# Performance work log

Measured on AMD Instinct MI355X. Metric: run time of the kernel, lower is better.

The kernel has to match this reference:

```python
import jax, jax.numpy as jnp
import numpy as np

B, L, D = 1, 1024, 1024
NL = 4            # n_layers
N = 16            # d_state
DI = 2 * D        # d_inner (expand=2)
DTR = (D + 15) // 16  # dt_rank = ceil(d_model/16) = 64
K = 4             # depthwise conv kernel size
EPS = 1e-5


def setup_inputs() -> dict:
    key = jax.random.key(0)
    ks = jax.random.split(key, 8)
    s = lambda k, shp, sc: jax.random.normal(k, shp, jnp.float32) * sc
    x = s(ks[0], (B, L, D), 1.0)
    norm_w = jnp.ones((NL, D), jnp.float32)
    in_w = s(ks[1], (NL, 2 * DI, D), D ** -0.5)          # in_proj (no bias)
    conv_w = s(ks[2], (NL, DI, K), 0.5)                   # depthwise conv1d weight
    conv_b = s(ks[3], (NL, DI), 0.02)                     # conv1d bias
    xproj_w = s(ks[4], (NL, DTR + 2 * N, DI), DI ** -0.5) # x_proj (no bias)
    dt_w = s(ks[5], (NL, DI, DTR), DTR ** -0.5)           # dt_proj weight
    dt_b = jnp.full((NL, DI), 0.1, jnp.float32)           # dt_proj bias (positive-ish delta)
    A_log = jnp.log(jnp.tile(jnp.arange(1, N + 1, dtype=jnp.float32), (NL, DI, 1)))  # [NL, DI, N]
    D_skip = jnp.ones((NL, DI), jnp.float32)
    out_w = s(ks[6], (NL, D, DI), DI ** -0.5)             # out_proj (no bias)
    return dict(x=x, norm_w=norm_w, in_w=in_w, conv_w=conv_w, conv_b=conv_b,
                xproj_w=xproj_w, dt_w=dt_w, dt_b=dt_b, A_log=A_log,
                D_skip=D_skip, out_w=out_w)


def _rmsnorm(x, w):
    return x * jax.lax.rsqrt(jnp.mean(x * x, axis=-1, keepdims=True) + EPS) * w


def _causal_depthwise_conv(u, w, b):
    # u: [B, L, DI], w: [DI, K], b: [DI]; causal (left pad K-1)
    up = jnp.pad(u, ((0, 0), (K - 1, 0), (0, 0)))
    y = b
    for k in range(K):
        y = y + up[:, k:k + L, :] * w[:, k]
    return y


def _selective_scan(dA, dBu, C):
    # dA, dBu: [B, L, DI, N]; C: [B, L, N]
    def step(h, inp):
        a, bu, c = inp
        h = a * h + bu                       # [B, DI, N]
        y = jnp.einsum('bdn,bn->bd', h, c)   # [B, DI]
        return h, y
    h0 = jnp.zeros((dA.shape[0], DI, N), dA.dtype)
    _, ys = jax.lax.scan(step, h0, (dA.transpose(1, 0, 2, 3),
                                    dBu.transpose(1, 0, 2, 3),
                                    C.transpose(1, 0, 2)))
    return ys.transpose(1, 0, 2)             # [B, L, DI]


def _mamba_block(x, p):
    norm_w, in_w, conv_w, conv_b, xproj_w, dt_w, dt_b, A_log, D_skip, out_w = p
    xn = _rmsnorm(x, norm_w)
    xz = jnp.einsum('bld,ed->ble', xn, in_w)             # [B, L, 2*DI]
    u, z = jnp.split(xz, 2, axis=-1)
    u = jax.nn.silu(_causal_depthwise_conv(u, conv_w, conv_b))
    x_dbl = jnp.einsum('bld,ed->ble', u, xproj_w)        # [B, L, DTR+2N]
    dt_r, Bt, Ct = jnp.split(x_dbl, [DTR, DTR + N], axis=-1)
    delta = jax.nn.softplus(jnp.einsum('blr,dr->bld', dt_r, dt_w) + dt_b)  # [B, L, DI]
    A = -jnp.exp(A_log)                                  # [DI, N]
    dA = jnp.exp(delta[..., None] * A)                   # [B, L, DI, N]
    dBu = delta[..., None] * Bt[:, :, None, :] * u[..., None]
    y = _selective_scan(dA, dBu, Ct) + u * D_skip        # [B, L, DI]
    y = y * jax.nn.silu(z)
    return x + jnp.einsum('ble,de->bld', y, out_w)       # residual


def reference(x, norm_w, in_w, conv_w, conv_b, xproj_w, dt_w, dt_b, A_log, D_skip, out_w):
    params = (norm_w, in_w, conv_w, conv_b, xproj_w, dt_w, dt_b, A_log, D_skip, out_w)
    out, _ = jax.lax.scan(lambda h, p: (_mamba_block(h, p), None), x, params)
    return out
```

## Files before the change

### kernel.cpp

```cpp
#include <hip/hip_runtime.h>
#include <hip/hip_bf16.h>
#include <stdint.h>

#define L 1024
#define D 1024
#define NLAYER 4
#define NSTATE 16
#define DI 2048
#define DTR 64
#define KCONV 4
#define XD 96
#define NC 64
#define CT 16
#define KSPLIT 8
#define OSPLIT 4
#define BK 32
#define DIST 4

typedef __attribute__((ext_vector_type(8))) short short8;
typedef __attribute__((ext_vector_type(4))) float floatx4;

__device__ __forceinline__ float siluf(float x) { return x / (1.f + __expf(-x)); }

__device__ __forceinline__ unsigned short f2bf(float x) {
    __hip_bfloat16 b = __float2bfloat16(x);
    return *reinterpret_cast<unsigned short*>(&b);
}

__device__ __forceinline__ short8 pack8(floatx4 a, floatx4 b) {
    short8 o;
    o[0] = (short)f2bf(a.x); o[1] = (short)f2bf(a.y);
    o[2] = (short)f2bf(a.z); o[3] = (short)f2bf(a.w);
    o[4] = (short)f2bf(b.x); o[5] = (short)f2bf(b.y);
    o[6] = (short)f2bf(b.z); o[7] = (short)f2bf(b.w);
    return o;
}

#define BARRIER_NODRAIN() asm volatile("s_waitcnt lgkmcnt(0)\n\ts_barrier" ::: "memory")

__global__ __launch_bounds__(256) void rmsnorm_kernel(const float* __restrict__ x,
                                                      const float* __restrict__ w,
                                                      __hip_bfloat16* __restrict__ out) {
    int row = blockIdx.x;
    const float* xr = x + (size_t)row * D;
    float v[4];
    float s = 0.f;
#pragma unroll
    for (int i = 0; i < 4; ++i) {
        v[i] = xr[threadIdx.x + i * 256];
        s += v[i] * v[i];
    }
#pragma unroll
    for (int off = 32; off > 0; off >>= 1) s += __shfl_xor(s, off, 64);
    __shared__ float red[4];
    int wave = threadIdx.x >> 6;
    if ((threadIdx.x & 63) == 0) red[wave] = s;
    __syncthreads();
    float tot = red[0] + red[1] + red[2] + red[3];
    float inv = rsqrtf(tot * (1.f / D) + 1e-5f);
#pragma unroll
    for (int i = 0; i < 4; ++i) {
        int c = threadIdx.x + i * 256;
        out[(size_t)row * D + c] = __float2bfloat16(v[i] * inv * w[c]);
    }
}

template <int EPI, int ITERS>
__global__ __launch_bounds__(256, 2) void gemm_pipe(
    const __hip_bfloat16* __restrict__ A, int lda,
    const float* __restrict__ Bw, int ldb, int Brows,
    float* __restrict__ C, int ldc, int Nvalid,
    long zstride, const float* __restrict__ bias) {
    __shared__ __align__(16) __hip_bfloat16 As[2][128 * BK];
    __shared__ __align__(16) __hip_bfloat16 Bs[2][64 * BK];
    int tid = threadIdx.x;
    int wave = tid >> 6, lane = tid & 63;

    int gxy = gridDim.x * gridDim.y;
    int total = gxy * gridDim.z;
    int flat = (blockIdx.z * gridDim.y + blockIdx.y) * gridDim.x + blockIdx.x;
    int bm, bn, bz;
    if ((total & 7) == 0) {
        int lid = (flat & 7) * (total >> 3) + (flat >> 3);
        bz = lid / gxy;
        int rem = lid - bz * gxy;
        bn = rem / gridDim.y;
        bm = rem - bn * gridDim.y;
    } else {
        bm = blockIdx.y; bn = blockIdx.x; bz = blockIdx.z;
    }

    int m0 = bm * 128, n0 = bn * 64;
    int k_base = bz * (ITERS * BK);
    C += (long)bz * zstride;
    int wr = wave >> 1, wc = wave & 1;
    int srow = lane >> 2, scol = (lane & 3) * 8;
    int q = lane >> 4, r = lane & 15;

    floatx4 acc[4][2] = {};

    const __hip_bfloat16* gA0 = A + (long)(m0 + wave * 32 + srow) * lda + scol + k_base;
    const __hip_bfloat16* gA1 = gA0 + (long)16 * lda;
    int bnrow = n0 + wave * 16 + srow;
    const float* gB = Bw + (long)bnrow * ldb + scol + k_base;
    bool bok = bnrow < Brows;

    short8 qa0[DIST], qa1[DIST];
    floatx4 qb0[DIST] = {}, qb1[DIST] = {};

    auto ld = [&](int j) {
        int k0 = j * BK;
        int s = j & (DIST - 1);
        qa0[s] = *(const short8*)(gA0 + k0);
        qa1[s] = *(const short8*)(gA1 + k0);
        if (bok) {
            qb0[s] = *(const floatx4*)(gB + k0);
            qb1[s] = *(const floatx4*)(gB + k0 + 4);
        }
    };
    auto wrstage = [&](int j) {
        int p = j & 1, s = j & (DIST - 1);
        *(short8*)(&As[p][(wave * 32 + srow) * BK + scol]) = qa0[s];
        *(short8*)(&As[p][(wave * 32 + 16 + srow) * BK + scol]) = qa1[s];
        *(short8*)(&Bs[p][(wave * 16 + srow) * BK + scol]) = pack8(qb0[s], qb1[s]);
    };

#pragma unroll
    for (int j = 0; j < DIST; ++j)
        if (j < ITERS) ld(j);
    wrstage(0);

#pragma unroll
    for (int k = 0; k < ITERS; ++k) {
        BARRIER_NODRAIN();
        if (k + DIST < ITERS) ld(k + DIST);
        if (k + 1 < ITERS) wrstage(k + 1);
        const short* Ap = (const short*)As[k & 1];
        const short* Bp = (const short*)Bs[k & 1];
        short8 af[4], bfr[2];
#pragma unroll
        for (int i = 0; i < 4; ++i)
            af[i] = *(const short8*)(Ap + (wr * 64 + i * 16 + r) * BK + q * 8);
#pragma unroll
        for (int j = 0; j < 2; ++j)
            bfr[j] = *(const short8*)(Bp + (wc * 32 + j * 16 + r) * BK + q * 8);
#pragma unroll
        for (int i = 0; i < 4; ++i)
#pragma unroll
            for (int j = 0; j < 2; ++j)
                acc[i][j] = __builtin_amdgcn_mfma_f32_16x16x32_bf16(af[i], bfr[j], acc[i][j], 0, 0, 0);
    }

#pragma unroll
    for (int i = 0; i < 4; ++i) {
        int mrow = m0 + wr * 64 + i * 16 + q * 4;
#pragma unroll
        for (int j = 0; j < 2; ++j) {
            int ncol = n0 + wc * 32 + j * 16 + r;
            if (ncol < Nvalid) {
#pragma unroll
                for (int rr = 0; rr < 4; ++rr) {
                    float v = acc[i][j][rr];
                    int m = mrow + rr;
                    if (EPI == 1) {
                        v += bias[ncol];
                        v = v > 20.f ? v : log1pf(__expf(v));
                    }
                    C[(long)m * ldc + ncol] = v;
                }
            }
        }
    }
}

template <int ITERS>
__global__ __launch_bounds__(256, 1) void gemm128(
    const __hip_bfloat16* __restrict__ A, int lda,
    const float* __restrict__ Bw, int ldb, int Brows,
    float* __restrict__ C, int ldc,
    long zstride) {
    __shared__ __align__(16) __hip_bfloat16 As[2][128 * BK];
    __shared__ __align__(16) __hip_bfloat16 Bs[2][128 * BK];
    int tid = threadIdx.x;
    int wave = tid >> 6, lane = tid & 63;

    int gxy = gridDim.x * gridDim.y;
    int total = gxy * gridDim.z;
    int flat = (blockIdx.z * gridDim.y + blockIdx.y) * gridDim.x + blockIdx.x;
    int bm, bn, bz;
    if ((total & 7) == 0) {
        int lid = (flat & 7) * (total >> 3) + (flat >> 3);
        bz = lid / gxy;
        int rem = lid - bz * gxy;
        bn = rem / gridDim.y;
        bm = rem - bn * gridDim.y;
    } else {
        bm = blockIdx.y; bn = blockIdx.x; bz = blockIdx.z;
    }

    int m0 = bm * 128, n0 = bn * 128;
    int k_base = bz * (ITERS * BK);
    C += (long)bz * zstride;
    int wr = wave >> 1, wc = wave & 1;
    int srow = lane >> 2, scol = (lane & 3) * 8;
    int q = lane >> 4, r = lane & 15;

    floatx4 acc[4][4] = {};

    const __hip_bfloat16* gA0 = A + (long)(m0 + wave * 32 + srow) * lda + scol + k_base;
    const __hip_bfloat16* gA1 = gA0 + (long)16 * lda;
    int bn0 = n0 + wave * 32 + srow;
    const float* gB0 = Bw + (long)bn0 * ldb + scol + k_base;
    const float* gB1 = gB0 + (long)16 * ldb;
    bool bok0 = bn0 < Brows, bok1 = (bn0 + 16) < Brows;

    short8 qa0[DIST], qa1[DIST];
    floatx4 qb0[DIST] = {}, qb1[DIST] = {}, qb2[DIST] = {}, qb3[DIST] = {};

    auto ld = [&](int j) {
        int k0 = j * BK;
        int s = j & (DIST - 1);
        qa0[s] = *(const short8*)(gA0 + k0);
        qa1[s] = *(const short8*)(gA1 + k0);
        if (bok0) {
            qb0[s] = *(const floatx4*)(gB0 + k0);
            qb1[s] = *(const floatx4*)(gB0 + k0 + 4);
        }
        if (bok1) {
            qb2[s] = *(const floatx4*)(gB1 + k0);
            qb3[s] = *(const floatx4*)(gB1 + k0 + 4);
        }
    };
    auto wrstage = [&](int j) {
        int p = j & 1, s = j & (DIST - 1);
        *(short8*)(&As[p][(wave * 32 + srow) * BK + scol]) = qa0[s];
        *(short8*)(&As[p][(wave * 32 + 16 + srow) * BK + scol]) = qa1[s];
        *(short8*)(&Bs[p][(wave * 32 + srow) * BK + scol]) = pack8(qb0[s], qb1[s]);
        *(short8*)(&Bs[p][(wave * 32 + 16 + srow) * BK + scol]) = pack8(qb2[s], qb3[s]);
    };

#pragma unroll
    for (int j = 0; j < DIST; ++j)
        if (j < ITERS) ld(j);
    wrstage(0);

#pragma unroll
    for (int k = 0; k < ITERS; ++k) {
        BARRIER_NODRAIN();
        if (k + DIST < ITERS) ld(k + DIST);
        if (k + 1 < ITERS) wrstage(k + 1);
        const short* Ap = (const short*)As[k & 1];
        const short* Bp = (const short*)Bs[k & 1];
        short8 af[4], bfr[4];
#pragma unroll
        for (int i = 0; i < 4; ++i)
            af[i] = *(const short8*)(Ap + (wr * 64 + i * 16 + r) * BK + q * 8);
#pragma unroll
        for (int j = 0; j < 4; ++j)
            bfr[j] = *(const short8*)(Bp + (wc * 64 + j * 16 + r) * BK + q * 8);
#pragma unroll
        for (int i = 0; i < 4; ++i)
#pragma unroll
            for (int j = 0; j < 4; ++j)
                acc[i][j] = __builtin_amdgcn_mfma_f32_16x16x32_bf16(af[i], bfr[j], acc[i][j], 0, 0, 0);
    }

#pragma unroll
    for (int i = 0; i < 4; ++i) {
        int mrow = m0 + wr * 64 + i * 16 + q * 4;
#pragma unroll
        for (int j = 0; j < 4; ++j) {
            int ncol = n0 + wc * 64 + j * 16 + r;
#pragma unroll
            for (int rr = 0; rr < 4; ++rr)
                C[(long)(mrow + rr) * ldc + ncol] = acc[i][j][rr];
        }
    }
}

template <int NPART, bool NORM>
__global__ __launch_bounds__(256) void reduce_kernel(const float* __restrict__ part2,
                                                     const float* __restrict__ xin,
                                                     const float* __restrict__ nw,
                                                     float* __restrict__ out,
                                                     __hip_bfloat16* __restrict__ xn) {
    int row = blockIdx.x;
    const float* xr = xin + (size_t)row * D;
    float v[4];
    float ss = 0.f;
#pragma unroll
    for (int i = 0; i < 4; ++i) {
        int c = threadIdx.x + i * 256;
        float s = xr[c];
#pragma unroll
        for (int p = 0; p < NPART; ++p)
            s += part2[(size_t)p * L * D + (size_t)row * D + c];
        v[i] = s;
        out[(size_t)row * D + c] = s;
        ss += s * s;
    }
    if (NORM) {
#pragma unroll
        for (int off = 32; off > 0; off >>= 1) ss += __shfl_xor(ss, off, 64);
        __shared__ float red[4];
        int wave = threadIdx.x >> 6;
        if ((threadIdx.x & 63) == 0) red[wave] = ss;
        __syncthreads();
        float inv = rsqrtf((red[0] + red[1] + red[2] + red[3]) * (1.f / D) + 1e-5f);
#pragma unroll
        for (int i = 0; i < 4; ++i) {
            int c = threadIdx.x + i * 256;
            xn[(size_t)row * D + c] = __float2bfloat16(v[i] * inv * nw[c]);
        }
    }
}

__global__ __launch_bounds__(256) void conv_silu_kernel(const float* __restrict__ xz,
                                                        const float* __restrict__ cw,
                                                        const float* __restrict__ cb,
                                                        __hip_bfloat16* __restrict__ u) {
    int idx = blockIdx.x * 256 + threadIdx.x;
    int d = idx & (DI - 1);
    int t = idx >> 11;
    float acc = cb[d];
#pragma unroll
    for (int k = 0; k < KCONV; ++k) {
        int tk = t - (KCONV - 1) + k;
        if (tk >= 0) acc += xz[(size_t)tk * (2 * DI) + d] * cw[d * KCONV + k];
    }
    u[idx] = __float2bfloat16(siluf(acc));
}

__global__ __launch_bounds__(256) void xred_kernel(const float* __restrict__ part,
                                                   __hip_bfloat16* __restrict__ xdbl_bf,
                                                   float* __restrict__ xdblBC) {
    int i = blockIdx.x * 256 + threadIdx.x;
    int t = i / XD, col = i - t * XD;
    float s = 0.f;
#pragma unroll
    for (int sp = 0; sp < KSPLIT; ++sp) s += part[(size_t)sp * L * XD + i];
    if (col < DTR) xdbl_bf[(size_t)t * DTR + col] = __float2bfloat16(s);
    else xdblBC[(size_t)t * 32 + (col - DTR)] = s;
}

__global__ __launch_bounds__(256) void scanA_kernel(const float* __restrict__ delta,
                                                    const __hip_bfloat16* __restrict__ u,
                                                    const float* __restrict__ xdblBC,
                                                    const float* __restrict__ Alog,
                                                    float* __restrict__ Ach,
                                                    float* __restrict__ Bch) {
    int d = blockIdx.x * 256 + threadIdx.x;
    int c = blockIdx.y;
    __shared__ __align__(16) float Bsh[CT * NSTATE];
    int tt0 = threadIdx.x >> 4, c0 = threadIdx.x & 15;
    Bsh[threadIdx.x] = xdblBC[(size_t)(c * CT + tt0) * 32 + c0];
    __syncthreads();

    float aval[NSTATE];
    const float4* Al4 = (const float4*)(Alog + (size_t)d * NSTATE);
#pragma unroll
    for (int n4 = 0; n4 < 4; ++n4) {
        float4 t = Al4[n4];
        aval[n4 * 4 + 0] = -__expf(t.x);
        aval[n4 * 4 + 1] = -__expf(t.y);
        aval[n4 * 4 + 2] = -__expf(t.z);
        aval[n4 * 4 + 3] = -__expf(t.w);
    }
    float h[NSTATE], ap[NSTATE];
#pragma unroll
    for (int n = 0; n < NSTATE; ++n) { h[n] = 0.f; ap[n] = 1.f; }

    for (int tt = 0; tt < CT; ++tt) {
        int t = c * CT + tt;
        float dl = delta[(size_t)t * DI + d];
        float uu = __bfloat162float(u[(size_t)t * DI + d]);
        float du = dl * uu;
        const float4* Bv = (const float4*)(Bsh + tt * NSTATE);
#pragma unroll
        for (int n4 = 0; n4 < 4; ++n4) {
            float4 b = Bv[n4];
            float bb[4] = {b.x, b.y, b.z, b.w};
#pragma unroll
            for (int k = 0; k < 4; ++k) {
                int n = n4 * 4 + k;
                float a = __expf(dl * aval[n]);
                h[n] = a * h[n] + du * bb[k];
                ap[n] *= a;
            }
        }
    }
    float4* Ao = (float4*)(Ach + ((size_t)c * DI + d) * NSTATE);
    float4* Bo = (float4*)(Bch + ((size_t)c * DI + d) * NSTATE);
#pragma unroll
    for (int n4 = 0; n4 < 4; ++n4) {
        Ao[n4] = make_float4(ap[n4 * 4], ap[n4 * 4 + 1], ap[n4 * 4 + 2], ap[n4 * 4 + 3]);
        Bo[n4] = make_float4(h[n4 * 4], h[n4 * 4 + 1], h[n4 * 4 + 2], h[n4 * 4 + 3]);
    }
}

__global__ __launch_bounds__(256) void scanB_kernel(float* __restrict__ Ach,
                                                    const float* __restrict__ Bch) {
    long i = blockIdx.x * 256 + threadIdx.x;
    const long S = (long)DI * NSTATE;
    constexpr int P = 8;
    float ab[P], bb[P];
#pragma unroll
    for (int j = 0; j < P; ++j) {
        ab[j] = Ach[(long)j * S + i];
        bb[j] = Bch[(long)j * S + i];
    }
    float h = 0.f;
#pragma unroll
    for (int c = 0; c < NC; ++c) {
        float a = ab[c & (P - 1)];
        float b = bb[c & (P - 1)];
        Ach[(long)c * S + i] = h;
        if (c + P < NC) {
            ab[c & (P - 1)] = Ach[(long)(c + P) * S + i];
            bb[c & (P - 1)] = Bch[(long)(c + P) * S + i];
        }
        h = a * h + b;
    }
}

__global__ __launch_bounds__(256) void scanC_kernel(const float* __restrict__ delta,
                                                    const __hip_bfloat16* __restrict__ u,
                                                    const float* __restrict__ xdblBC,
                                                    const float* __restrict__ Alog,
                                                    const float* __restrict__ Hin,
                                                    const float* __restrict__ xz,
                                                    const float* __restrict__ Dskip,
                                                    __hip_bfloat16* __restrict__ yg) {
    int d = blockIdx.x * 256 + threadIdx.x;
    int c = blockIdx.y;
    __shared__ __align__(16) float Bsh[CT * NSTATE];
    __shared__ __align__(16) float Csh[CT * NSTATE];
    int tt0 = threadIdx.x >> 4, c0 = threadIdx.x & 15;
    Bsh[threadIdx.x] = xdblBC[(size_t)(c * CT + tt0) * 32 + c0];
    Csh[threadIdx.x] = xdblBC[(size_t)(c * CT + tt0) * 32 + 16 + c0];
    __syncthreads();

    float aval[NSTATE];
    const float4* Al4 = (const float4*)(Alog + (size_t)d * NSTATE);
#pragma unroll
    for (int n4 = 0; n4 < 4; ++n4) {
        float4 t = Al4[n4];
        aval[n4 * 4 + 0] = -__expf(t.x);
        aval[n4 * 4 + 1] = -__expf(t.y);
        aval[n4 * 4 + 2] = -__expf(t.z);
        aval[n4 * 4 + 3] = -__expf(t.w);
    }
    float h[NSTATE];
    const float4* Hi = (const float4*)(Hin + ((size_t)c * DI + d) * NSTATE);
#pragma unroll
    for (int n4 = 0; n4 < 4; ++n4) {
        float4 t = Hi[n4];
        h[n4 * 4 + 0] = t.x; h[n4 * 4 + 1] = t.y; h[n4 * 4 + 2] = t.z; h[n4 * 4 + 3] = t.w;
    }
    float dsk = Dskip[d];

    for (int tt = 0; tt < CT; ++tt) {
        int t = c * CT + tt;
        float dl = delta[(size_t)t * DI + d];
        float uu = __bfloat162float(u[(size_t)t * DI + d]);
        float du = dl * uu;
        const float4* Bv = (const float4*)(Bsh + tt * NSTATE);
        const float4* Cv = (const float4*)(Csh + tt * NSTATE);
        float y = 0.f;
#pragma unroll
        for (int n4 = 0; n4 < 4; ++n4) {
            float4 b = Bv[n4];
            float4 cc = Cv[n4];
            float bb[4] = {b.x, b.y, b.z, b.w};
            float cv[4] = {cc.x, cc.y, cc.z, cc.w};
#pragma unroll
            for (int k = 0; k < 4; ++k) {
                int n = n4 * 4 + k;
                float a = __expf(dl * aval[n]);
                h[n] = a * h[n] + du * bb[k];
                y += h[n] * cv[k];
            }
        }
        float z = xz[(size_t)t * (2 * DI) + DI + d];
        yg[(size_t)t * DI + d] = __float2bfloat16((y + uu * dsk) * siluf(z));
    }
}

extern "C" void kernel_launch(void* const* d_in, const int* in_sizes, int n_in,
                              void* d_out, int out_size, void* d_ws, size_t ws_size,
                              hipStream_t stream) {
    const float* x      = (const float*)d_in[0];
    const float* norm_w = (const float*)d_in[1];
    const float* in_w   = (const float*)d_in[2];
    const float* conv_w = (const float*)d_in[3];
    const float* conv_b = (const float*)d_in[4];
    const float* xproj_w= (const float*)d_in[5];
    const float* dt_w   = (const float*)d_in[6];
    const float* dt_b   = (const float*)d_in[7];
    const float* A_log  = (const float*)d_in[8];
    const float* D_skip = (const float*)d_in[9];
    const float* out_w  = (const float*)d_in[10];
    float* out = (float*)d_out;

    uint8_t* wp = (uint8_t*)d_ws;
    auto alloc = [&](size_t bytes) {
        uint8_t* p = wp;
        wp += (bytes + 255) & ~(size_t)255;
        return p;
    };
    __hip_bfloat16* xn_bf   = (__hip_bfloat16*)alloc((size_t)L * D * 2);
    float*          xz      = (float*)alloc((size_t)L * 2 * DI * 4);
    __hip_bfloat16* u_bf    = (__hip_bfloat16*)alloc((size_t)L * DI * 2);
    float*          part    = (float*)alloc((size_t)KSPLIT * L * XD * 4);
    __hip_bfloat16* xdbl_bf = (__hip_bfloat16*)alloc((size_t)L * DTR * 2);
    float*          xdblBC  = (float*)alloc((size_t)L * 32 * 4);
    float*          delta   = (float*)alloc((size_t)L * DI * 4);
    __hip_bfloat16* yg_bf   = (__hip_bfloat16*)alloc((size_t)L * DI * 2);
    float*          part2   = (float*)alloc((size_t)OSPLIT * L * D * 4);
    float*          Ach     = (float*)alloc((size_t)NC * DI * NSTATE * 4);
    float*          Bch     = (float*)alloc((size_t)NC * DI * NSTATE * 4);

    rmsnorm_kernel<<<L, 256, 0, stream>>>(x, norm_w, xn_bf);

    for (int l = 0; l < NLAYER; ++l) {
        const float* xin = (l == 0) ? x : out;

        gemm128<32><<<dim3(4096 / 128, L / 128, 1), 256, 0, stream>>>(
            xn_bf, D, in_w + (size_t)l * 4096 * 1024, D, 4096,
            xz, 4096, 0);

        conv_silu_kernel<<<L * DI / 256, 256, 0, stream>>>(
            xz, conv_w + (size_t)l * DI * KCONV, conv_b + (size_t)l * DI, u_bf);

        gemm_pipe<0, 8><<<dim3(2, L / 128, KSPLIT), 256, 0, stream>>>(
            u_bf, DI, xproj_w + (size_t)l * 96 * 2048, DI, 96,
            part, XD, XD, (long)L * XD, nullptr);
        xred_kernel<<<(L * XD) / 256, 256, 0, stream>>>(part, xdbl_bf, xdblBC);

        gemm_pipe<1, 2><<<dim3(2048 / 64, L / 128, 1), 256, 0, stream>>>(
            xdbl_bf, DTR, dt_w + (size_t)l * 2048 * 64, DTR, 2048,
            delta, DI, DI, 0, dt_b + (size_t)l * DI);

        scanA_kernel<<<dim3(DI / 256, NC), 256, 0, stream>>>(
            delta, u_bf, xdblBC, A_log + (size_t)l * DI * NSTATE, Ach, Bch);
        scanB_kernel<<<(DI * NSTATE) / 256, 256, 0, stream>>>(Ach, Bch);
        scanC_kernel<<<dim3(DI / 256, NC), 256, 0, stream>>>(
            delta, u_bf, xdblBC, A_log + (size_t)l * DI * NSTATE, Ach, xz,
            D_skip + (size_t)l * DI, yg_bf);

        gemm128<16><<<dim3(1024 / 128, L / 128, OSPLIT), 256, 0, stream>>>(
            yg_bf, DI, out_w + (size_t)l * 1024 * 2048, DI, 1024,
            part2, D, (long)L * D);

        if (l < NLAYER - 1)
            reduce_kernel<OSPLIT, true><<<L, 256, 0, stream>>>(
                part2, xin, norm_w + (size_t)(l + 1) * D, out, xn_bf);
        else
            reduce_kernel<OSPLIT, false><<<L, 256, 0, stream>>>(
                part2, xin, nullptr, out, nullptr);
    }
}
```

Before: 598.7 us.

## Replace three-pass chunked selective scan with single sequential fused scan kernel

Replaces the chunked scan (a per-chunk local scan, a cross-chunk carry pass and a re-scan with output) with one kernel. Each block owns 32 channels and walks all 1024 timesteps in order, with 8 lanes per channel each holding 2 states. Delta, u, z and B/C are double-buffered through LDS in 64-step tiles, and lanes are reduced with shuffles. This removes the redundant exponentials, the Ach/Bch traffic and two launches. In exchange only 64 blocks run and each carries a long serial dependency chain, so the scan becomes latency-bound with low occupancy.

After: 1.230 ms. 2.05x slower.

```diff
diff --git a/kernel.cpp b/kernel.cpp
--- a/kernel.cpp
+++ b/kernel.cpp
@@ -10,12 +10,12 @@
 #define DTR 64
 #define KCONV 4
 #define XD 96
-#define NC 64
-#define CT 16
 #define KSPLIT 8
 #define OSPLIT 4
 #define BK 32
 #define DIST 4
+#define SCAND 32
+#define TT 64
 
 typedef __attribute__((ext_vector_type(8))) short short8;
 typedef __attribute__((ext_vector_type(4))) float floatx4;
@@ -56,8 +56,7 @@
     int wave = threadIdx.x >> 6;
     if ((threadIdx.x & 63) == 0) red[wave] = s;
     __syncthreads();
-    float tot = red[0] + red[1] + red[2] + red[3];
-    float inv = rsqrtf(tot * (1.f / D) + 1e-5f);
+    float inv = rsqrtf((red[0] + red[1] + red[2] + red[3]) * (1.f / D) + 1e-5f);
 #pragma unroll
     for (int i = 0; i < 4; ++i) {
         int c = threadIdx.x + i * 256;
@@ -177,8 +176,7 @@
 __global__ __launch_bounds__(256, 1) void gemm128(
     const __hip_bfloat16* __restrict__ A, int lda,
     const float* __restrict__ Bw, int ldb, int Brows,
-    float* __restrict__ C, int ldc,
-    long zstride) {
+    float* __restrict__ C, int ldc, long zstride) {
     __shared__ __align__(16) __hip_bfloat16 As[2][128 * BK];
     __shared__ __align__(16) __hip_bfloat16 Bs[2][128 * BK];
     int tid = threadIdx.x;
@@ -343,146 +341,82 @@
     else xdblBC[(size_t)t * 32 + (col - DTR)] = s;
 }
 
-__global__ __launch_bounds__(256) void scanA_kernel(const float* __restrict__ delta,
-                                                    const __hip_bfloat16* __restrict__ u,
-                                                    const float* __restrict__ xdblBC,
-                                                    const float* __restrict__ Alog,
-                                                    float* __restrict__ Ach,
-                                                    float* __restrict__ Bch) {
-    int d = blockIdx.x * 256 + threadIdx.x;
-    int c = blockIdx.y;
-    __shared__ __align__(16) float Bsh[CT * NSTATE];
-    int tt0 = threadIdx.x >> 4, c0 = threadIdx.x & 15;
-    Bsh[threadIdx.x] = xdblBC[(size_t)(c * CT + tt0) * 32 + c0];
-    __syncthreads();
-
-    float aval[NSTATE];
-    const float4* Al4 = (const float4*)(Alog + (size_t)d * NSTATE);
-#pragma unroll
-    for (int n4 = 0; n4 < 4; ++n4) {
-        float4 t = Al4[n4];
-        aval[n4 * 4 + 0] = -__expf(t.x);
-        aval[n4 * 4 + 1] = -__expf(t.y);
-        aval[n4 * 4 + 2] = -__expf(t.z);
-        aval[n4 * 4 + 3] = -__expf(t.w);
-    }
-    float h[NSTATE], ap[NSTATE];
-#pragma unroll
-    for (int n = 0; n < NSTATE; ++n) { h[n] = 0.f; ap[n] = 1.f; }
-
-    for (int tt = 0; tt < CT; ++tt) {
-        int t = c * CT + tt;
-        float dl = delta[(size_t)t * DI + d];
-        float uu = __bfloat162float(u[(size_t)t * DI + d]);
-        float du = dl * uu;
-        const float4* Bv = (const float4*)(Bsh + tt * NSTATE);
-#pragma unroll
-        for (int n4 = 0; n4 < 4; ++n4) {
-            float4 b = Bv[n4];
-            float bb[4] = {b.x, b.y, b.z, b.w};
-#pragma unroll
-            for (int k = 0; k < 4; ++k) {
-                int n = n4 * 4 + k;
-                float a = __expf(dl * aval[n]);
-                h[n] = a * h[n] + du * bb[k];
-                ap[n] *= a;
-            }
-        }
-    }
-    float4* Ao = (float4*)(Ach + ((size_t)c * DI + d) * NSTATE);
-    float4* Bo = (float4*)(Bch + ((size_t)c * DI + d) * NSTATE);
-#pragma unroll
-    for (int n4 = 0; n4 < 4; ++n4) {
-        Ao[n4] = make_float4(ap[n4 * 4], ap[n4 * 4 + 1], ap[n4 * 4 + 2], ap[n4 * 4 + 3]);
-        Bo[n4] = make_float4(h[n4 * 4], h[n4 * 4 + 1], h[n4 * 4 + 2], h[n4 * 4 + 3]);
-    }
-}
-
-__global__ __launch_bounds__(256) void scanB_kernel(float* __restrict__ Ach,
-                                                    const float* __restrict__ Bch) {
-    long i = blockIdx.x * 256 + threadIdx.x;
-    const long S = (long)DI * NSTATE;
-    constexpr int P = 8;
-    float ab[P], bb[P];
-#pragma unroll
-    for (int j = 0; j < P; ++j) {
-        ab[j] = Ach[(long)j * S + i];
-        bb[j] = Bch[(long)j * S + i];
-    }
-    float h = 0.f;
-#pragma unroll
-    for (int c = 0; c < NC; ++c) {
-        float a = ab[c & (P - 1)];
-        float b = bb[c & (P - 1)];
-        Ach[(long)c * S + i] = h;
-        if (c + P < NC) {
-            ab[c & (P - 1)] = Ach[(long)(c + P) * S + i];
-            bb[c & (P - 1)] = Bch[(long)(c + P) * S + i];
-        }
-        h = a * h + b;
-    }
-}
-
-__global__ __launch_bounds__(256) void scanC_kernel(const float* __restrict__ delta,
-                                                    const __hip_bfloat16* __restrict__ u,
-                                                    const float* __restrict__ xdblBC,
-                                                    const float* __restrict__ Alog,
-                                                    const float* __restrict__ Hin,
-                                                    const float* __restrict__ xz,
-                                                    const float* __restrict__ Dskip,
-                                                    __hip_bfloat16* __restrict__ yg) {
-    int d = blockIdx.x * 256 + threadIdx.x;
-    int c = blockIdx.y;
-    __shared__ __align__(16) float Bsh[CT * NSTATE];
-    __shared__ __align__(16) float Csh[CT * NSTATE];
-    int tt0 = threadIdx.x >> 4, c0 = threadIdx.x & 15;
-    Bsh[threadIdx.x] = xdblBC[(size_t)(c * CT + tt0) * 32 + c0];
-    Csh[threadIdx.x] = xdblBC[(size_t)(c * CT + tt0) * 32 + 16 + c0];
-    __syncthreads();
-
-    float aval[NSTATE];
-    const float4* Al4 = (const float4*)(Alog + (size_t)d * NSTATE);
-#pragma unroll
-    for (int n4 = 0; n4 < 4; ++n4) {
-        float4 t = Al4[n4];
-        aval[n4 * 4 + 0] = -__expf(t.x);
-        aval[n4 * 4 + 1] = -__expf(t.y);
-        aval[n4 * 4 + 2] = -__expf(t.z);
-        aval[n4 * 4 + 3] = -__expf(t.w);
-    }
-    float h[NSTATE];
-    const float4* Hi = (const float4*)(Hin + ((size_t)c * DI + d) * NSTATE);
-#pragma unroll
-    for (int n4 = 0; n4 < 4; ++n4) {
-        float4 t = Hi[n4];
-        h[n4 * 4 + 0] = t.x; h[n4 * 4 + 1] = t.y; h[n4 * 4 + 2] = t.z; h[n4 * 4 + 3] = t.w;
-    }
-    float dsk = Dskip[d];
-
-    for (int tt = 0; tt < CT; ++tt) {
-        int t = c * CT + tt;
-        float dl = delta[(size_t)t * DI + d];
-        float uu = __bfloat162float(u[(size_t)t * DI + d]);
-        float du = dl * uu;
-        const float4* Bv = (const float4*)(Bsh + tt * NSTATE);
-        const float4* Cv = (const float4*)(Csh + tt * NSTATE);
-        float y = 0.f;
-#pragma unroll
-        for (int n4 = 0; n4 < 4; ++n4) {
-            float4 b = Bv[n4];
-            float4 cc = Cv[n4];
-            float bb[4] = {b.x, b.y, b.z, b.w};
-            float cv[4] = {cc.x, cc.y, cc.z, cc.w};
-#pragma unroll
-            for (int k = 0; k < 4; ++k) {
-                int n = n4 * 4 + k;
-                float a = __expf(dl * aval[n]);
-                h[n] = a * h[n] + du * bb[k];
-                y += h[n] * cv[k];
-            }
-        }
-        float z = xz[(size_t)t * (2 * DI) + DI + d];
-        yg[(size_t)t * DI + d] = __float2bfloat16((y + uu * dsk) * siluf(z));
+__global__ __launch_bounds__(256) void scan1_kernel(
+    const float* __restrict__ delta, const __hip_bfloat16* __restrict__ u,
+    const float* __restrict__ xdblBC, const float* __restrict__ Alog,
+    const float* __restrict__ xz, const float* __restrict__ Dskip,
+    __hip_bfloat16* __restrict__ yg) {
+    const int d0 = blockIdx.x * SCAND;
+    const int tid = threadIdx.x;
+    const int dl_ = tid >> 3;
+    const int ng = tid & 7;
+    const int d = d0 + dl_;
+    const int n0 = ng * 2;
+
+    __shared__ __align__(16) float dsl[2][TT * SCAND];
+    __shared__ __align__(16) float usl[2][TT * SCAND];
+    __shared__ __align__(16) float zsl[2][TT * SCAND];
+    __shared__ __align__(16) float bcs[2][TT * 32];
+    __shared__ __align__(16) float ysl[TT * SCAND];
+    __shared__ float dskL[SCAND];
+
+    if (tid < SCAND) dskL[tid] = Dskip[d0 + tid];
+
+    float av0 = -__expf(Alog[(size_t)d * NSTATE + n0]);
+    float av1 = -__expf(Alog[(size_t)d * NSTATE + n0 + 1]);
+    float h0 = 0.f, h1 = 0.f;
+
+    auto stage = [&](int b, int tile) {
+        int T0 = tile * TT;
+#pragma unroll
+        for (int i = 0; i < (TT * SCAND) / 256; ++i) {
+            int idx = i * 256 + tid;
+            int tt = idx >> 5, col = idx & 31;
+            int t = T0 + tt;
+            dsl[b][idx] = delta[(size_t)t * DI + d0 + col];
+            usl[b][idx] = __bfloat162float(u[(size_t)t * DI + d0 + col]);
+            zsl[b][idx] = xz[(size_t)t * (2 * DI) + DI + d0 + col];
+            bcs[b][idx] = xdblBC[(size_t)t * 32 + col];
+        }
+    };
+
+    stage(0, 0);
+    for (int tile = 0; tile < L / TT; ++tile) {
+        int b = tile & 1;
+        __syncthreads();
+        if (tile + 1 < L / TT) stage(b ^ 1, tile + 1);
+#pragma unroll 4
+        for (int tt = 0; tt < TT; ++tt) {
+            float dlv = dsl[b][tt * SCAND + dl_];
+            float uu  = usl[b][tt * SCAND + dl_];
+            float du  = dlv * uu;
+            float bb0 = bcs[b][tt * 32 + n0];
+            float bb1 = bcs[b][tt * 32 + n0 + 1];
+            float cc0 = bcs[b][tt * 32 + 16 + n0];
+            float cc1 = bcs[b][tt * 32 + 16 + n0 + 1];
+            float a0 = __expf(dlv * av0);
+            float a1 = __expf(dlv * av1);
+            h0 = a0 * h0 + du * bb0;
+            h1 = a1 * h1 + du * bb1;
+            float y = h0 * cc0 + h1 * cc1;
+            y += __shfl_xor(y, 1);
+            y += __shfl_xor(y, 2);
+            y += __shfl_xor(y, 4);
+            if (ng == 0) ysl[tt * SCAND + dl_] = y;
+        }
+        __syncthreads();
+        int T0 = tile * TT;
+#pragma unroll
+        for (int i = 0; i < (TT * SCAND) / 256; ++i) {
+            int idx = i * 256 + tid;
+            int tt = idx >> 5, col = idx & 31;
+            int t = T0 + tt;
+            float y = ysl[idx];
+            float uu = usl[b][idx];
+            float z = zsl[b][idx];
+            yg[(size_t)t * DI + d0 + col] =
+                __float2bfloat16((y + uu * dskL[col]) * siluf(z));
+        }
     }
 }
 
@@ -517,8 +451,6 @@
     float*          delta   = (float*)alloc((size_t)L * DI * 4);
     __hip_bfloat16* yg_bf   = (__hip_bfloat16*)alloc((size_t)L * DI * 2);
     float*          part2   = (float*)alloc((size_t)OSPLIT * L * D * 4);
-    float*          Ach     = (float*)alloc((size_t)NC * DI * NSTATE * 4);
-    float*          Bch     = (float*)alloc((size_t)NC * DI * NSTATE * 4);
 
     rmsnorm_kernel<<<L, 256, 0, stream>>>(x, norm_w, xn_bf);
 
@@ -526,8 +458,7 @@
         const float* xin = (l == 0) ? x : out;
 
         gemm128<32><<<dim3(4096 / 128, L / 128, 1), 256, 0, stream>>>(
-            xn_bf, D, in_w + (size_t)l * 4096 * 1024, D, 4096,
-            xz, 4096, 0);
+            xn_bf, D, in_w + (size_t)l * 4096 * 1024, D, 4096, xz, 4096, 0);
 
         conv_silu_kernel<<<L * DI / 256, 256, 0, stream>>>(
             xz, conv_w + (size_t)l * DI * KCONV, conv_b + (size_t)l * DI, u_bf);
@@ -541,14 +472,11 @@
             xdbl_bf, DTR, dt_w + (size_t)l * 2048 * 64, DTR, 2048,
             delta, DI, DI, 0, dt_b + (size_t)l * DI);
 
-        scanA_kernel<<<dim3(DI / 256, NC), 256, 0, stream>>>(
-            delta, u_bf, xdblBC, A_log + (size_t)l * DI * NSTATE, Ach, Bch);
-        scanB_kernel<<<(DI * NSTATE) / 256, 256, 0, stream>>>(Ach, Bch);
-        scanC_kernel<<<dim3(DI / 256, NC), 256, 0, stream>>>(
-            delta, u_bf, xdblBC, A_log + (size_t)l * DI * NSTATE, Ach, xz,
+        scan1_kernel<<<DI / SCAND, 256, 0, stream>>>(
+            delta, u_bf, xdblBC, A_log + (size_t)l * DI * NSTATE, xz,
             D_skip + (size_t)l * DI, yg_bf);
 
-        gemm128<16><<<dim3(1024 / 128, L / 128, OSPLIT), 256, 0, stream>>>(
+        gemm128<2048 / (OSPLIT * BK)><<<dim3(1024 / 128, L / 128, OSPLIT), 256, 0, stream>>>(
             yg_bf, DI, out_w + (size_t)l * 1024 * 2048, DI, 1024,
             part2, D, (long)L * D);
 
```
